# Kernel tuning notes

Hardware: AMD Instinct MI355X
Metric: run time of the kernel (lower is better)

Reference implementation:

```python
import jax, jax.numpy as jnp
import numpy as np

D_PROJ = 256
SCALE = D_PROJ ** (-0.5)


def setup_inputs() -> dict:
    key = jax.random.key(0)
    k1, k2, k3, k4 = jax.random.split(key, 4)
    B, L, Dh = 16, 2048, 1280
    T, Dg = 512, 768
    H = jax.random.normal(k1, (B, L, Dh), dtype=jnp.float32)
    G = jax.random.normal(k2, (B, T, Dg), dtype=jnp.float32)
    # Linear weights (torch nn.Linear: out = x @ W.T), small init to keep softmax well-conditioned
    Wq = jax.random.normal(k3, (D_PROJ, Dg), dtype=jnp.float32) * 0.02
    Wk = jax.random.normal(k4, (D_PROJ, Dh), dtype=jnp.float32) * 0.02
    return {"H": H, "G": G, "Wq": Wq, "Wk": Wk}


def reference(H, G, Wq, Wk):
    # Q = Wq(G): [B,T,P]; K = Wk(H): [B,L,P]
    Q = jnp.einsum('btg,pg->btp', G, Wq)
    K = jnp.einsum('bld,pd->blp', H, Wk)
    # The torch module's chunked online-softmax computes exact softmax over L.
    logits = jnp.einsum('btp,blp->btl', Q, K) * SCALE  # [B,T,L]
    A = jax.nn.softmax(logits, axis=-1)
    # Values are the raw residue embeddings H (not projected).
    Z = jnp.einsum('btl,bld->btd', A, H)  # [B,T,Dh]
    return Z
```

## Files before the change

### kernel.cpp

```cpp
#include <hip/hip_runtime.h>
#include <stdint.h>

typedef __attribute__((ext_vector_type(8))) short   short8;
typedef __attribute__((ext_vector_type(8))) __bf16  bf16x8;
typedef __attribute__((ext_vector_type(4))) float   floatx4;

#define DEV static __device__ __forceinline__

DEV unsigned short f2b(float f) {
  union { float f; unsigned u; } v; v.f = f;
  unsigned u = v.u;
  unsigned r = u + 0x7FFFu + ((u >> 16) & 1u);
  return (unsigned short)(r >> 16);
}

DEV void gload_lds16(const void* g, void* l) {
  __builtin_amdgcn_global_load_lds(
      (const __attribute__((address_space(1))) unsigned int*)g,
      (__attribute__((address_space(3))) unsigned int*)l,
      16, 0, 0);
}

__global__ void cvt3_kernel(const float* __restrict__ a, unsigned short* __restrict__ oa, int na4,
                            const float* __restrict__ b, unsigned short* __restrict__ ob, int nb4,
                            const float* __restrict__ c, unsigned short* __restrict__ oc, int nc4) {
  int i = blockIdx.x * blockDim.x + threadIdx.x;
  const float* src; unsigned short* dst; int k;
  if (i < na4)                { src = a; dst = oa; k = i; }
  else if (i < na4 + nb4)     { src = b; dst = ob; k = i - na4; }
  else if (i < na4 + nb4 + nc4) { src = c; dst = oc; k = i - na4 - nb4; }
  else return;
  float4 v = ((const float4*)src)[k];
  ushort4 o;
  o.x = f2b(v.x); o.y = f2b(v.y); o.z = f2b(v.z); o.w = f2b(v.w);
  ((ushort4*)dst)[k] = o;
}

__global__ void zero_kernel(float* __restrict__ p, int n) {
  int i = blockIdx.x * blockDim.x + threadIdx.x;
  if (i < n) p[i] = 0.f;
}

__global__ void transpose_cvt_H(const float* __restrict__ H, unsigned short* __restrict__ HT) {
  __shared__ unsigned short tile[64 * 66];
  const int b  = blockIdx.z;
  const int l0 = blockIdx.x * 64;
  const int d0 = blockIdx.y * 64;
  const int t  = threadIdx.x;

  {
    int row = t >> 2;
    int seg = t & 3;
    const float* src = H + ((size_t)b * 2048 + l0 + row) * 1280 + d0 + seg * 16;
    unsigned short* trow = &tile[row * 66 + seg * 16];
#pragma unroll
    for (int s = 0; s < 4; ++s) {
      float4 v = *(const float4*)(src + s * 4);
      ushort2 p0 = { f2b(v.x), f2b(v.y) };
      ushort2 p1 = { f2b(v.z), f2b(v.w) };
      *(ushort2*)&trow[s * 4]     = p0;
      *(ushort2*)&trow[s * 4 + 2] = p1;
    }
  }
  __syncthreads();
  {
    int dr = t >> 2;
    int ls = (t & 3) * 16;
    unsigned short* dst = HT + ((size_t)b * 1280 + d0 + dr) * 2048 + l0 + ls;
    short8 a, c;
#pragma unroll
    for (int i = 0; i < 8; ++i) a[i] = (short)tile[(ls + i) * 66 + dr];
#pragma unroll
    for (int i = 0; i < 8; ++i) c[i] = (short)tile[(ls + 8 + i) * 66 + dr];
    *(short8*)dst = a;
    *(short8*)(dst + 8) = c;
  }
}

template <int AMODE>
__global__ void proj_gemm(const void* __restrict__ Apv, const unsigned short* __restrict__ Bt,
                          unsigned short* __restrict__ C, int K, int lda) {
  __shared__ unsigned short As[64 * 32];
  __shared__ unsigned short Bs[256 * 32];

  const int m0   = blockIdx.x * 64;
  const int t    = threadIdx.x;
  const int lane = t & 63;
  const int wave = t >> 6;
  const int wn   = wave * 64;
  const int r16  = lane & 15;
  const int q    = lane >> 4;

  const unsigned short* Abf = (const unsigned short*)Apv;
  const float* A32 = (const float*)Apv;

  floatx4 acc[4][4];
#pragma unroll
  for (int i = 0; i < 4; ++i)
#pragma unroll
    for (int j = 0; j < 4; ++j) acc[i][j] = (floatx4){0.f, 0.f, 0.f, 0.f};

  for (int kt = 0; kt < K; kt += 32) {
    __syncthreads();
#pragma unroll
    for (int cc = 0; cc < 4; ++cc) {
      int c = t + cc * 256;
      gload_lds16(Bt + (size_t)(c >> 2) * K + kt + (c & 3) * 8, &Bs[c * 8]);
    }
    if constexpr (AMODE == 0) {
      gload_lds16(Abf + (size_t)(m0 + (t >> 2)) * lda + kt + (t & 3) * 8, &As[t * 8]);
    } else {
      const float* g = A32 + (size_t)(m0 + (t >> 2)) * lda + kt + (t & 3) * 8;
      float4 v0 = *(const float4*)g;
      float4 v1 = *(const float4*)(g + 4);
      short8 p;
      p[0] = (short)f2b(v0.x); p[1] = (short)f2b(v0.y);
      p[2] = (short)f2b(v0.z); p[3] = (short)f2b(v0.w);
      p[4] = (short)f2b(v1.x); p[5] = (short)f2b(v1.y);
      p[6] = (short)f2b(v1.z); p[7] = (short)f2b(v1.w);
      *(short8*)&As[t * 8] = p;
    }
    __syncthreads();

    bf16x8 af[4], bfr[4];
#pragma unroll
    for (int i = 0; i < 4; ++i) af[i]  = *(const bf16x8*)&As[(i * 16 + r16) * 32 + q * 8];
#pragma unroll
    for (int j = 0; j < 4; ++j) bfr[j] = *(const bf16x8*)&Bs[(wn + j * 16 + r16) * 32 + q * 8];
#pragma unroll
    for (int i = 0; i < 4; ++i)
#pragma unroll
      for (int j = 0; j < 4; ++j)
        acc[i][j] = __builtin_amdgcn_mfma_f32_16x16x32_bf16(af[i], bfr[j], acc[i][j], 0, 0, 0);
  }

#pragma unroll
  for (int i = 0; i < 4; ++i) {
#pragma unroll
    for (int r = 0; r < 4; ++r) {
      int m = m0 + i * 16 + q * 4 + r;
#pragma unroll
      for (int j = 0; j < 4; ++j) {
        int n = wn + j * 16 + r16;
        C[(size_t)m * 256 + n] = f2b(acc[i][j][r]);
      }
    }
  }
}

template <int EPI>
__global__ void gemm_nt(const unsigned short* __restrict__ Ab, const unsigned short* __restrict__ Btb,
                        void* __restrict__ Cpv, float* __restrict__ sums,
                        int K, int lda, int ldb, int ldc,
                        long long sA, long long sB, long long sC, int sstride,
                        float escale, int nx, int tiles_pb) {
  __shared__ unsigned short As[128 * 32];
  __shared__ unsigned short Bs[128 * 32];

  const int g   = blockIdx.x;
  const int xcd = g & 7;
  const int jj  = g >> 3;
  const int bz  = xcd * 2 + jj / tiles_pb;
  const int tt  = jj % tiles_pb;
  const int m0  = (tt / nx) * 128;
  const int n0  = (tt % nx) * 128;

  const int t    = threadIdx.x;
  const int lane = t & 63;
  const int wave = t >> 6;
  const int wm   = (wave & 1) * 64;
  const int wn   = (wave >> 1) * 64;
  const int r16  = lane & 15;
  const int q    = lane >> 4;

  const unsigned short* Bt = Btb + (long long)bz * sB;
  const unsigned short* A  = Ab + (long long)bz * sA;

  floatx4 acc[4][4];
#pragma unroll
  for (int i = 0; i < 4; ++i)
#pragma unroll
    for (int j = 0; j < 4; ++j) acc[i][j] = (floatx4){0.f, 0.f, 0.f, 0.f};

  for (int kt = 0; kt < K; kt += 32) {
    __syncthreads();
#pragma unroll
    for (int cc = 0; cc < 2; ++cc) {
      int c = t + cc * 256;
      gload_lds16(Bt + (size_t)(n0 + (c >> 2)) * ldb + kt + (c & 3) * 8, &Bs[c * 8]);
    }
#pragma unroll
    for (int cc = 0; cc < 2; ++cc) {
      int c = t + cc * 256;
      gload_lds16(A + (size_t)(m0 + (c >> 2)) * lda + kt + (c & 3) * 8, &As[c * 8]);
    }
    __syncthreads();

    bf16x8 af[4], bfr[4];
#pragma unroll
    for (int i = 0; i < 4; ++i) af[i]  = *(const bf16x8*)&As[(wm + i * 16 + r16) * 32 + q * 8];
#pragma unroll
    for (int j = 0; j < 4; ++j) bfr[j] = *(const bf16x8*)&Bs[(wn + j * 16 + r16) * 32 + q * 8];
#pragma unroll
    for (int i = 0; i < 4; ++i)
#pragma unroll
      for (int j = 0; j < 4; ++j)
        acc[i][j] = __builtin_amdgcn_mfma_f32_16x16x32_bf16(af[i], bfr[j], acc[i][j], 0, 0, 0);
  }

  if constexpr (EPI == 1) {
    unsigned short* C = (unsigned short*)Cpv + (long long)bz * sC;
#pragma unroll
    for (int i = 0; i < 4; ++i) {
#pragma unroll
      for (int r = 0; r < 4; ++r) {
        int m = m0 + wm + i * 16 + q * 4 + r;
        float ps = 0.f;
#pragma unroll
        for (int j = 0; j < 4; ++j) {
          int n = n0 + wn + j * 16 + r16;
          float v = __expf(acc[i][j][r] * escale);
          ps += v;
          C[(size_t)m * ldc + n] = f2b(v);
        }
#pragma unroll
        for (int msk = 1; msk < 16; msk <<= 1) ps += __shfl_xor(ps, msk, 64);
        if (r16 == 0) atomicAdd(&sums[(long long)bz * sstride + m], ps);
      }
    }
  } else {
    float* C = (float*)Cpv + (long long)bz * sC;
    const float* sb = sums + (long long)bz * sstride;
#pragma unroll
    for (int i = 0; i < 4; ++i) {
#pragma unroll
      for (int r = 0; r < 4; ++r) {
        int m = m0 + wm + i * 16 + q * 4 + r;
        float sc = 1.0f / sb[m];
#pragma unroll
        for (int j = 0; j < 4; ++j) {
          int n = n0 + wn + j * 16 + r16;
          C[(size_t)m * ldc + n] = acc[i][j][r] * sc;
        }
      }
    }
  }
}

extern "C" void kernel_launch(void* const* d_in, const int* in_sizes, int n_in,
                              void* d_out, int out_size, void* d_ws, size_t ws_size,
                              hipStream_t stream) {
  (void)in_sizes; (void)n_in; (void)out_size; (void)ws_size;
  const float* H  = (const float*)d_in[0];
  const float* G  = (const float*)d_in[1];
  const float* Wq = (const float*)d_in[2];
  const float* Wk = (const float*)d_in[3];
  float* Z = (float*)d_out;

  constexpr int B = 16, L = 2048, Dh = 1280, T = 512, Dg = 768, P = 256;

  char* ws = (char*)d_ws;
  size_t off = 0;
  auto alloc = [&](size_t bytes) { void* p = ws + off; off += (bytes + 255) & ~(size_t)255; return p; };
  unsigned short* Gbf  = (unsigned short*)alloc((size_t)B * T * Dg * 2);
  unsigned short* Wqbf = (unsigned short*)alloc((size_t)P * Dg * 2);
  unsigned short* Wkbf = (unsigned short*)alloc((size_t)P * Dh * 2);
  unsigned short* Qbf  = (unsigned short*)alloc((size_t)B * T * P * 2);
  unsigned short* Kbf  = (unsigned short*)alloc((size_t)B * L * P * 2);
  unsigned short* HT   = (unsigned short*)alloc((size_t)B * Dh * L * 2);
  unsigned short* E    = (unsigned short*)alloc((size_t)B * T * L * 2);
  float*          sums = (float*)alloc((size_t)B * T * 4);

  {
    int na4 = B * T * Dg / 4, nb4 = P * Dg / 4, nc4 = P * Dh / 4;
    cvt3_kernel<<<(na4 + nb4 + nc4 + 255) / 256, 256, 0, stream>>>(
        G, Gbf, na4, Wq, Wqbf, nb4, Wk, Wkbf, nc4);
  }
  zero_kernel<<<(B * T + 255) / 256, 256, 0, stream>>>(sums, B * T);
  transpose_cvt_H<<<dim3(L / 64, Dh / 64, B), 256, 0, stream>>>(H, HT);

  proj_gemm<0><<<B * T / 64, 256, 0, stream>>>(Gbf, Wqbf, Qbf, Dg, Dg);
  proj_gemm<1><<<B * L / 64, 256, 0, stream>>>(H, Wkbf, Kbf, Dh, Dh);

  gemm_nt<1><<<B * (T / 128) * (L / 128), 256, 0, stream>>>(
      Qbf, Kbf, E, sums, P, P, P, L,
      (long long)T * P, (long long)L * P, (long long)T * L, T,
      0.0625f, L / 128, (T / 128) * (L / 128));

  gemm_nt<2><<<B * (T / 128) * (Dh / 128), 256, 0, stream>>>(
      E, HT, Z, sums, L, L, L, Dh,
      (long long)T * L, (long long)Dh * L, (long long)T * Dh, T,
      0.f, Dh / 128, (T / 128) * (Dh / 128));
}
```

Baseline: 444.2 us.

## Fuse H transpose-convert into K projection GEMM and drop standalone G conversion

The separate transpose_cvt_H kernel is removed. The K-projection GEMM, which already loads H as fp32 and converts it to bf16 in LDS, now writes the transposed bf16 tile HT out of that LDS buffer. The Q projection reads fp32 G directly instead of a pre-converted bf16 copy, and the zeroing of sums is folded into the weight-conversion kernel. This avoids a second full read of H and the G round trip and cuts kernel launches, at the cost of extra LDS reads and strided global stores inside the projection loop.

```diff
diff --git a/kernel.cpp b/kernel.cpp
--- a/kernel.cpp
+++ b/kernel.cpp
@@ -21,65 +21,28 @@
       16, 0, 0);
 }
 
-__global__ void cvt3_kernel(const float* __restrict__ a, unsigned short* __restrict__ oa, int na4,
+__global__ void cvtw_kernel(const float* __restrict__ a, unsigned short* __restrict__ oa, int na4,
                             const float* __restrict__ b, unsigned short* __restrict__ ob, int nb4,
-                            const float* __restrict__ c, unsigned short* __restrict__ oc, int nc4) {
+                            float* __restrict__ zp, int nz) {
   int i = blockIdx.x * blockDim.x + threadIdx.x;
-  const float* src; unsigned short* dst; int k;
-  if (i < na4)                { src = a; dst = oa; k = i; }
-  else if (i < na4 + nb4)     { src = b; dst = ob; k = i - na4; }
-  else if (i < na4 + nb4 + nc4) { src = c; dst = oc; k = i - na4 - nb4; }
-  else return;
-  float4 v = ((const float4*)src)[k];
-  ushort4 o;
-  o.x = f2b(v.x); o.y = f2b(v.y); o.z = f2b(v.z); o.w = f2b(v.w);
-  ((ushort4*)dst)[k] = o;
-}
-
-__global__ void zero_kernel(float* __restrict__ p, int n) {
-  int i = blockIdx.x * blockDim.x + threadIdx.x;
-  if (i < n) p[i] = 0.f;
-}
-
-__global__ void transpose_cvt_H(const float* __restrict__ H, unsigned short* __restrict__ HT) {
-  __shared__ unsigned short tile[64 * 66];
-  const int b  = blockIdx.z;
-  const int l0 = blockIdx.x * 64;
-  const int d0 = blockIdx.y * 64;
-  const int t  = threadIdx.x;
-
-  {
-    int row = t >> 2;
-    int seg = t & 3;
-    const float* src = H + ((size_t)b * 2048 + l0 + row) * 1280 + d0 + seg * 16;
-    unsigned short* trow = &tile[row * 66 + seg * 16];
-#pragma unroll
-    for (int s = 0; s < 4; ++s) {
-      float4 v = *(const float4*)(src + s * 4);
-      ushort2 p0 = { f2b(v.x), f2b(v.y) };
-      ushort2 p1 = { f2b(v.z), f2b(v.w) };
-      *(ushort2*)&trow[s * 4]     = p0;
-      *(ushort2*)&trow[s * 4 + 2] = p1;
-    }
-  }
-  __syncthreads();
-  {
-    int dr = t >> 2;
-    int ls = (t & 3) * 16;
-    unsigned short* dst = HT + ((size_t)b * 1280 + d0 + dr) * 2048 + l0 + ls;
-    short8 a, c;
-#pragma unroll
-    for (int i = 0; i < 8; ++i) a[i] = (short)tile[(ls + i) * 66 + dr];
-#pragma unroll
-    for (int i = 0; i < 8; ++i) c[i] = (short)tile[(ls + 8 + i) * 66 + dr];
-    *(short8*)dst = a;
-    *(short8*)(dst + 8) = c;
-  }
-}
-
-template <int AMODE>
-__global__ void proj_gemm(const void* __restrict__ Apv, const unsigned short* __restrict__ Bt,
-                          unsigned short* __restrict__ C, int K, int lda) {
+  if (i < na4) {
+    float4 v = ((const float4*)a)[i];
+    ushort4 o; o.x = f2b(v.x); o.y = f2b(v.y); o.z = f2b(v.z); o.w = f2b(v.w);
+    ((ushort4*)oa)[i] = o;
+  } else if (i < na4 + nb4) {
+    int k = i - na4;
+    float4 v = ((const float4*)b)[k];
+    ushort4 o; o.x = f2b(v.x); o.y = f2b(v.y); o.z = f2b(v.z); o.w = f2b(v.w);
+    ((ushort4*)ob)[k] = o;
+  } else if (i < na4 + nb4 + nz) {
+    zp[i - na4 - nb4] = 0.f;
+  }
+}
+
+template <int WRITE_HT>
+__global__ void proj_gemm(const float* __restrict__ A32, const unsigned short* __restrict__ Bt,
+                          unsigned short* __restrict__ C, unsigned short* __restrict__ HT,
+                          int K, int lda) {
   __shared__ unsigned short As[64 * 32];
   __shared__ unsigned short Bs[256 * 32];
 
@@ -91,9 +54,6 @@
   const int r16  = lane & 15;
   const int q    = lane >> 4;
 
-  const unsigned short* Abf = (const unsigned short*)Apv;
-  const float* A32 = (const float*)Apv;
-
   floatx4 acc[4][4];
 #pragma unroll
   for (int i = 0; i < 4; ++i)
@@ -107,9 +67,7 @@
       int c = t + cc * 256;
       gload_lds16(Bt + (size_t)(c >> 2) * K + kt + (c & 3) * 8, &Bs[c * 8]);
     }
-    if constexpr (AMODE == 0) {
-      gload_lds16(Abf + (size_t)(m0 + (t >> 2)) * lda + kt + (t & 3) * 8, &As[t * 8]);
-    } else {
+    {
       const float* g = A32 + (size_t)(m0 + (t >> 2)) * lda + kt + (t & 3) * 8;
       float4 v0 = *(const float4*)g;
       float4 v1 = *(const float4*)(g + 4);
@@ -132,6 +90,17 @@
 #pragma unroll
       for (int j = 0; j < 4; ++j)
         acc[i][j] = __builtin_amdgcn_mfma_f32_16x16x32_bf16(af[i], bfr[j], acc[i][j], 0, 0, 0);
+
+    if constexpr (WRITE_HT) {
+      const int d  = t >> 3;
+      const int lc = t & 7;
+      short8 v;
+#pragma unroll
+      for (int j = 0; j < 8; ++j) v[j] = (short)As[(lc * 8 + j) * 32 + d];
+      const int b  = m0 >> 11;
+      const int l0 = m0 & 2047;
+      *(short8*)&HT[((size_t)b * 1280 + kt + d) * 2048 + l0 + lc * 8] = v;
+    }
   }
 
 #pragma unroll
@@ -262,7 +231,6 @@
   char* ws = (char*)d_ws;
   size_t off = 0;
   auto alloc = [&](size_t bytes) { void* p = ws + off; off += (bytes + 255) & ~(size_t)255; return p; };
-  unsigned short* Gbf  = (unsigned short*)alloc((size_t)B * T * Dg * 2);
   unsigned short* Wqbf = (unsigned short*)alloc((size_t)P * Dg * 2);
   unsigned short* Wkbf = (unsigned short*)alloc((size_t)P * Dh * 2);
   unsigned short* Qbf  = (unsigned short*)alloc((size_t)B * T * P * 2);
@@ -272,15 +240,13 @@
   float*          sums = (float*)alloc((size_t)B * T * 4);
 
   {
-    int na4 = B * T * Dg / 4, nb4 = P * Dg / 4, nc4 = P * Dh / 4;
-    cvt3_kernel<<<(na4 + nb4 + nc4 + 255) / 256, 256, 0, stream>>>(
-        G, Gbf, na4, Wq, Wqbf, nb4, Wk, Wkbf, nc4);
-  }
-  zero_kernel<<<(B * T + 255) / 256, 256, 0, stream>>>(sums, B * T);
-  transpose_cvt_H<<<dim3(L / 64, Dh / 64, B), 256, 0, stream>>>(H, HT);
-
-  proj_gemm<0><<<B * T / 64, 256, 0, stream>>>(Gbf, Wqbf, Qbf, Dg, Dg);
-  proj_gemm<1><<<B * L / 64, 256, 0, stream>>>(H, Wkbf, Kbf, Dh, Dh);
+    int na4 = P * Dg / 4, nb4 = P * Dh / 4, nz = B * T;
+    cvtw_kernel<<<(na4 + nb4 + nz + 255) / 256, 256, 0, stream>>>(
+        Wq, Wqbf, na4, Wk, Wkbf, nb4, sums, nz);
+  }
+
+  proj_gemm<0><<<B * T / 64, 256, 0, stream>>>(G, Wqbf, Qbf, nullptr, Dg, Dg);
+  proj_gemm<1><<<B * L / 64, 256, 0, stream>>>(H, Wkbf, Kbf, HT, Dh, Dh);
 
   gemm_nt<1><<<B * (T / 128) * (L / 128), 256, 0, stream>>>(
       Qbf, Kbf, E, sums, P, P, P, L,
```

Result: faster. 412.0 us (-7.2%).
